# Kernel optimization log

Measured on AMD Instinct MI355X. Metric: run time of the kernel, lower is better.

## Reference

```python
import jax, jax.numpy as jnp
import numpy as np

NUM_HEADS = 16
HEAD_SIZE = 64
LN_EPS = 1e-5


def setup_inputs() -> dict:
    key = jax.random.key(0)
    k1, k2, k3 = jax.random.split(key, 3)
    b, l, hidden = 2, 2048, 1024
    qkv_out = HEAD_SIZE * NUM_HEADS + 2 * HEAD_SIZE  # 1152
    x = jax.random.normal(k1, (b, l, hidden), dtype=jnp.float32)
    Wqkv = jax.random.normal(k2, (qkv_out, hidden), dtype=jnp.float32) * 0.02
    gamma = jnp.ones((qkv_out,), dtype=jnp.float32)
    beta = jnp.zeros((qkv_out,), dtype=jnp.float32)
    Wfc = jax.random.normal(k3, (hidden, HEAD_SIZE * NUM_HEADS), dtype=jnp.float32) * 0.02
    return {"x": x, "Wqkv": Wqkv, "gamma": gamma, "beta": beta, "Wfc": Wfc}


def reference(x, Wqkv, gamma, beta, Wfc):
    h, d = NUM_HEADS, HEAD_SIZE
    b, l, _ = x.shape
    # fused QKV projection (no bias), then LayerNorm over the FULL qkv dim
    qkv = jnp.einsum('blc,oc->blo', x, Wqkv)  # (b, l, (h+2)*d)
    mu = jnp.mean(qkv, axis=-1, keepdims=True)
    var = jnp.var(qkv, axis=-1, keepdims=True)
    qkv = (qkv - mu) * jax.lax.rsqrt(var + LN_EPS) * gamma + beta
    qkv = qkv.reshape(b, l, h + 2, d)
    k = qkv[:, :, 0, :]       # (b, l, d) shared K head
    v = qkv[:, :, 1, :]       # (b, l, d) shared V head
    q = qkv[:, :, 2:, :]      # (b, l, h, d) query heads
    scale = 1.0 / np.sqrt(d).astype(np.float32)
    scores = jnp.einsum('bqhd,bkd->bhqk', q, k) * scale  # (b, h, l, l)
    causal = jnp.tril(jnp.ones((l, l), dtype=bool))
    scores = jnp.where(causal, scores, jnp.finfo(scores.dtype).min)
    attn = jax.nn.softmax(scores, axis=-1)
    out = jnp.einsum('bhqk,bkd->bqhd', attn, v).reshape(b, l, h * d)
    return jnp.einsum('blo,ho->blh', out, Wfc)
```

## Files before the change

kernel.cpp:

```cpp
#include <hip/hip_runtime.h>
#include <stdint.h>

typedef __attribute__((ext_vector_type(8))) short s16x8;
typedef __attribute__((ext_vector_type(4))) float f32x4;

#define MFMA16(a, b, c) __builtin_amdgcn_mfma_f32_16x16x32_bf16((a), (b), (c), 0, 0, 0)

__device__ __forceinline__ unsigned short f2bf(float f) {
    unsigned int u = __float_as_uint(f);
    return (unsigned short)((u + 0x7FFFu + ((u >> 16) & 1u)) >> 16);
}
__device__ __forceinline__ float bf2f(unsigned short h) {
    return __uint_as_float(((unsigned int)h) << 16);
}
__device__ __forceinline__ void cvt8(unsigned short* dst, const float* src) {
    const float4 f0 = *(const float4*)(src);
    const float4 f1 = *(const float4*)(src + 4);
    s16x8 v;
    v[0] = (short)f2bf(f0.x); v[1] = (short)f2bf(f0.y);
    v[2] = (short)f2bf(f0.z); v[3] = (short)f2bf(f0.w);
    v[4] = (short)f2bf(f1.x); v[5] = (short)f2bf(f1.y);
    v[6] = (short)f2bf(f1.z); v[7] = (short)f2bf(f1.w);
    *(s16x8*)dst = v;
}
__device__ __forceinline__ void gl_lds16(const unsigned short* g, unsigned short* l) {
    __builtin_amdgcn_global_load_lds(
        (const __attribute__((address_space(1))) unsigned int*)g,
        (__attribute__((address_space(3))) unsigned int*)l,
        16, 0, 0);
}

__global__ __launch_bounds__(256) void cvt_all(const float* __restrict__ x,
                                               const float* __restrict__ wq,
                                               const float* __restrict__ wf,
                                               unsigned short* __restrict__ xb,
                                               unsigned short* __restrict__ wqb,
                                               unsigned short* __restrict__ wfb) {
    const int blk = blockIdx.x;
    const float* src;
    unsigned short* dst;
    int base;
    if (blk < 2048)      { src = x;  dst = xb;  base = blk; }
    else if (blk < 2624) { src = wq; dst = wqb; base = blk - 2048; }
    else                 { src = wf; dst = wfb; base = blk - 2624; }
    const int i = (base * 256 + threadIdx.x) * 8;
    cvt8(&dst[i], &src[i]);
}

template <bool OUT_F32>
__global__ __launch_bounds__(256) void gemm_mn(const unsigned short* __restrict__ A,
                                               const unsigned short* __restrict__ Bw,
                                               void* __restrict__ Cout, int K, int N) {
    const int bm = blockIdx.x, bn = blockIdx.y;
    const int t = threadIdx.x;
    const int lane = t & 63, w = t >> 6;
    const int quad = lane >> 4, col = lane & 15;
    const int wm = (w >> 1) * 64, wn = (w & 1) * 32;

    __shared__ alignas(16) unsigned short As[128 * 64];
    __shared__ alignas(16) unsigned short Bs[64 * 64];

    f32x4 acc[4][2];
#pragma unroll
    for (int i = 0; i < 4; ++i)
#pragma unroll
        for (int j = 0; j < 2; ++j) acc[i][j] = (f32x4){0.f, 0.f, 0.f, 0.f};

    const int lrow = lane >> 3;
    const int lcol = (lane & 7) * 8;
    const unsigned short* Ap = A + (size_t)(bm * 128 + w * 8 + lrow) * K + lcol;
    const unsigned short* Bp = Bw + (size_t)(bn * 64 + w * 8 + lrow) * K + lcol;

    for (int k0 = 0; k0 < K; k0 += 64) {
        __syncthreads();
#pragma unroll
        for (int j = 0; j < 4; ++j)
            gl_lds16(Ap + (size_t)(j * 32) * K + k0, &As[(j * 32 + w * 8) * 64]);
#pragma unroll
        for (int j = 0; j < 2; ++j)
            gl_lds16(Bp + (size_t)(j * 32) * K + k0, &Bs[(j * 32 + w * 8) * 64]);
        __syncthreads();
#pragma unroll
        for (int s = 0; s < 2; ++s) {
            s16x8 af[4], bfr[2];
#pragma unroll
            for (int i = 0; i < 4; ++i)
                af[i] = *(const s16x8*)&As[(wm + i * 16 + col) * 64 + s * 32 + quad * 8];
#pragma unroll
            for (int j = 0; j < 2; ++j)
                bfr[j] = *(const s16x8*)&Bs[(wn + j * 16 + col) * 64 + s * 32 + quad * 8];
#pragma unroll
            for (int i = 0; i < 4; ++i)
#pragma unroll
                for (int j = 0; j < 2; ++j)
                    acc[i][j] = MFMA16(af[i], bfr[j], acc[i][j]);
        }
    }
    const int rowb = bm * 128 + wm + quad * 4;
    const int colb = bn * 64 + wn + col;
#pragma unroll
    for (int i = 0; i < 4; ++i)
#pragma unroll
        for (int j = 0; j < 2; ++j)
#pragma unroll
            for (int r = 0; r < 4; ++r) {
                size_t off = (size_t)(rowb + i * 16 + r) * N + colb + j * 16;
                if (OUT_F32) ((float*)Cout)[off] = acc[i][j][r];
                else ((unsigned short*)Cout)[off] = f2bf(acc[i][j][r]);
            }
}

__global__ __launch_bounds__(256) void ln_split(unsigned short* __restrict__ qkvn,
                                                const float* __restrict__ gamma,
                                                const float* __restrict__ beta,
                                                unsigned short* __restrict__ vT) {
    const int row = blockIdx.x;
    const int b = row >> 11, l = row & 2047;
    unsigned short* rp = qkvn + (size_t)row * 1152;
    const int t = threadIdx.x;
    const bool act = t < 144;

    float fv[8];
    float s = 0.f, s2 = 0.f;
    if (act) {
        s16x8 v = *(const s16x8*)&rp[t * 8];
#pragma unroll
        for (int e = 0; e < 8; ++e) {
            fv[e] = bf2f((unsigned short)v[e]);
            s += fv[e];
            s2 += fv[e] * fv[e];
        }
    } else {
#pragma unroll
        for (int e = 0; e < 8; ++e) fv[e] = 0.f;
    }
#pragma unroll
    for (int off = 32; off; off >>= 1) {
        s += __shfl_down(s, off);
        s2 += __shfl_down(s2, off);
    }
    __shared__ float red[8];
    const int lane = t & 63, w = t >> 6;
    if (lane == 0) { red[w] = s; red[w + 4] = s2; }
    __syncthreads();
    s = red[0] + red[1] + red[2] + red[3];
    s2 = red[4] + red[5] + red[6] + red[7];
    const float mu = s * (1.0f / 1152.0f);
    float var = s2 * (1.0f / 1152.0f) - mu * mu;
    var = fmaxf(var, 0.0f);
    const float rstd = rsqrtf(var + 1e-5f);

    if (act) {
        float4 g0 = *(const float4*)&gamma[t * 8];
        float4 g1 = *(const float4*)&gamma[t * 8 + 4];
        float4 e0 = *(const float4*)&beta[t * 8];
        float4 e1 = *(const float4*)&beta[t * 8 + 4];
        const float gg[8] = {g0.x, g0.y, g0.z, g0.w, g1.x, g1.y, g1.z, g1.w};
        const float bb[8] = {e0.x, e0.y, e0.z, e0.w, e1.x, e1.y, e1.z, e1.w};
        s16x8 o;
#pragma unroll
        for (int e = 0; e < 8; ++e)
            o[e] = (short)f2bf((fv[e] - mu) * rstd * gg[e] + bb[e]);
        *(s16x8*)&rp[t * 8] = o;
        if (t >= 8 && t < 16) {
            const int d0 = t * 8 - 64;
#pragma unroll
            for (int e = 0; e < 8; ++e)
                vT[((size_t)(b * 64 + d0 + e)) * 2048 + l] = (unsigned short)o[e];
        }
    }
}

__global__ __launch_bounds__(512) void attn_kernel(const unsigned short* __restrict__ qkvn,
                                                   const unsigned short* __restrict__ vT,
                                                   unsigned short* __restrict__ obuf) {
    const int b = blockIdx.x >> 3, hp = blockIdx.x & 7;
    const int qb = 31 - blockIdx.y;
    const int t = threadIdx.x;
    const int lane = t & 63, w = t >> 6;
    const int quad = lane >> 4, col = lane & 15;
    const int hl = w >> 2, wq = w & 3;

    __shared__ alignas(16) unsigned short Ks[2][64][72];
    __shared__ alignas(16) unsigned short Vts[2][64][72];
    __shared__ alignas(16) unsigned short PQ[8][16][72];

    unsigned short(*Qs)[72] = (unsigned short(*)[72])PQ;

    const int rs = t >> 3;
    const int cs = (t & 7) * 8;

#pragma unroll
    for (int hh = 0; hh < 2; ++hh) {
        const unsigned short* qsrc =
            qkvn + (size_t)(b * 2048 + qb * 64 + rs) * 1152 + 128 + (hp * 2 + hh) * 64 + cs;
        s16x8 v = *(const s16x8*)qsrc;
#pragma unroll
        for (int e = 0; e < 8; ++e)
            v[e] = (short)f2bf(bf2f((unsigned short)v[e]) * 0.125f);
        *(s16x8*)&Qs[hh * 64 + rs][cs] = v;
    }
    __syncthreads();
    const s16x8 qf0 = *(const s16x8*)&Qs[hl * 64 + wq * 16 + col][quad * 8];
    const s16x8 qf1 = *(const s16x8*)&Qs[hl * 64 + wq * 16 + col][32 + quad * 8];

    const unsigned short* kbase = qkvn + (size_t)(b * 2048 + rs) * 1152 + cs;
    const unsigned short* vbase = vT + (size_t)(b * 64 + rs) * 2048 + cs;
    *(uint4*)&Ks[0][rs][cs]  = *(const uint4*)(kbase);
    *(uint4*)&Vts[0][rs][cs] = *(const uint4*)(vbase);
    __syncthreads();

    s16x8 ones;
#pragma unroll
    for (int e = 0; e < 8; ++e) ones[e] = (short)0x3F80;

    f32x4 Oacc[4];
    f32x4 lacc = {0.f, 0.f, 0.f, 0.f};
#pragma unroll
    for (int nt = 0; nt < 4; ++nt) Oacc[nt] = (f32x4){0.f, 0.f, 0.f, 0.f};

    const int qg = qb * 64 + wq * 16 + quad * 4;

    for (int kb = 0; kb <= qb; ++kb) {
        const int p = kb & 1;
        uint4 kreg, vreg;
        if (kb < qb) {
            kreg = *(const uint4*)(kbase + (size_t)(kb + 1) * 64 * 1152);
            vreg = *(const uint4*)(vbase + (kb + 1) * 64);
        }

        f32x4 S[4];
#pragma unroll
        for (int nt = 0; nt < 4; ++nt) {
            s16x8 kf0 = *(const s16x8*)&Ks[p][nt * 16 + col][quad * 8];
            s16x8 kf1 = *(const s16x8*)&Ks[p][nt * 16 + col][32 + quad * 8];
            f32x4 z = (f32x4){0.f, 0.f, 0.f, 0.f};
            z = MFMA16(qf0, kf0, z);
            z = MFMA16(qf1, kf1, z);
            S[nt] = z;
        }
        if (kb == qb) {
#pragma unroll
            for (int nt = 0; nt < 4; ++nt)
#pragma unroll
                for (int r = 0; r < 4; ++r)
                    if (kb * 64 + nt * 16 + col > qg + r) S[nt][r] = -1e30f;
        }

#pragma unroll
        for (int nt = 0; nt < 4; ++nt)
#pragma unroll
            for (int r = 0; r < 4; ++r)
                PQ[w][quad * 4 + r][nt * 16 + col] = f2bf(__expf(S[nt][r] - 12.0f));

        const s16x8 pf0 = *(const s16x8*)&PQ[w][col][quad * 8];
        const s16x8 pf1 = *(const s16x8*)&PQ[w][col][32 + quad * 8];
        lacc = MFMA16(pf0, ones, lacc);
        lacc = MFMA16(pf1, ones, lacc);
#pragma unroll
        for (int nt = 0; nt < 4; ++nt) {
            s16x8 vf0 = *(const s16x8*)&Vts[p][nt * 16 + col][quad * 8];
            s16x8 vf1 = *(const s16x8*)&Vts[p][nt * 16 + col][32 + quad * 8];
            Oacc[nt] = MFMA16(pf0, vf0, Oacc[nt]);
            Oacc[nt] = MFMA16(pf1, vf1, Oacc[nt]);
        }

        if (kb < qb) {
            *(uint4*)&Ks[p ^ 1][rs][cs]  = kreg;
            *(uint4*)&Vts[p ^ 1][rs][cs] = vreg;
        }
        __syncthreads();
    }

    const int h = hp * 2 + hl;
#pragma unroll
    for (int r = 0; r < 4; ++r) {
        float inv = 1.0f / lacc[r];
        size_t base = (((size_t)b * 2048 + qg + r) * 16 + h) * 64;
#pragma unroll
        for (int nt = 0; nt < 4; ++nt)
            obuf[base + nt * 16 + col] = f2bf(Oacc[nt][r] * inv);
    }
}

extern "C" void kernel_launch(void* const* d_in, const int* in_sizes, int n_in,
                              void* d_out, int out_size, void* d_ws, size_t ws_size,
                              hipStream_t stream) {
    (void)in_sizes; (void)n_in; (void)out_size; (void)ws_size;
    const float* x     = (const float*)d_in[0];
    const float* Wqkv  = (const float*)d_in[1];
    const float* gamma = (const float*)d_in[2];
    const float* beta  = (const float*)d_in[3];
    const float* Wfc   = (const float*)d_in[4];
    float* out = (float*)d_out;

    char* ws = (char*)d_ws;
    unsigned short* xb   = (unsigned short*)ws;
    unsigned short* Wqb  = (unsigned short*)(ws + 8388608);
    unsigned short* Wfb  = (unsigned short*)(ws + 10747904);
    unsigned short* qkvn = (unsigned short*)(ws + 12845056);
    unsigned short* vT   = (unsigned short*)(ws + 22282240);
    unsigned short* abuf = (unsigned short*)ws;

    cvt_all<<<dim3(3136), 256, 0, stream>>>(x, Wqkv, Wfc, xb, Wqb, Wfb);
    gemm_mn<false><<<dim3(32, 18), 256, 0, stream>>>(xb, Wqb, qkvn, 1024, 1152);
    ln_split<<<dim3(4096), 256, 0, stream>>>(qkvn, gamma, beta, vT);
    attn_kernel<<<dim3(16, 32), 512, 0, stream>>>(qkvn, vT, abuf);
    gemm_mn<true><<<dim3(32, 16), 256, 0, stream>>>(abuf, Wfb, out, 1024, 1024);
}
```

Measured before the change: 172.7 us.

## Double-buffer GEMM LDS tiles and use single-wave LayerNorm rows

```diff
diff --git a/kernel.cpp b/kernel.cpp
--- a/kernel.cpp
+++ b/kernel.cpp
@@ -57,8 +57,8 @@
     const int quad = lane >> 4, col = lane & 15;
     const int wm = (w >> 1) * 64, wn = (w & 1) * 32;
 
-    __shared__ alignas(16) unsigned short As[128 * 64];
-    __shared__ alignas(16) unsigned short Bs[64 * 64];
+    __shared__ alignas(16) unsigned short As[2][128 * 64];
+    __shared__ alignas(16) unsigned short Bs[2][64 * 64];
 
     f32x4 acc[4][2];
 #pragma unroll
@@ -71,30 +71,40 @@
     const unsigned short* Ap = A + (size_t)(bm * 128 + w * 8 + lrow) * K + lcol;
     const unsigned short* Bp = Bw + (size_t)(bn * 64 + w * 8 + lrow) * K + lcol;
 
+#pragma unroll
+    for (int j = 0; j < 4; ++j)
+        gl_lds16(Ap + (size_t)(j * 32) * K, &As[0][(j * 32 + w * 8) * 64]);
+#pragma unroll
+    for (int j = 0; j < 2; ++j)
+        gl_lds16(Bp + (size_t)(j * 32) * K, &Bs[0][(j * 32 + w * 8) * 64]);
+    __syncthreads();
+
     for (int k0 = 0; k0 < K; k0 += 64) {
-        __syncthreads();
-#pragma unroll
-        for (int j = 0; j < 4; ++j)
-            gl_lds16(Ap + (size_t)(j * 32) * K + k0, &As[(j * 32 + w * 8) * 64]);
-#pragma unroll
-        for (int j = 0; j < 2; ++j)
-            gl_lds16(Bp + (size_t)(j * 32) * K + k0, &Bs[(j * 32 + w * 8) * 64]);
-        __syncthreads();
+        const int p = (k0 >> 6) & 1;
+        if (k0 + 64 < K) {
+#pragma unroll
+            for (int j = 0; j < 4; ++j)
+                gl_lds16(Ap + (size_t)(j * 32) * K + k0 + 64, &As[p ^ 1][(j * 32 + w * 8) * 64]);
+#pragma unroll
+            for (int j = 0; j < 2; ++j)
+                gl_lds16(Bp + (size_t)(j * 32) * K + k0 + 64, &Bs[p ^ 1][(j * 32 + w * 8) * 64]);
+        }
 #pragma unroll
         for (int s = 0; s < 2; ++s) {
             s16x8 af[4], bfr[2];
 #pragma unroll
             for (int i = 0; i < 4; ++i)
-                af[i] = *(const s16x8*)&As[(wm + i * 16 + col) * 64 + s * 32 + quad * 8];
+                af[i] = *(const s16x8*)&As[p][(wm + i * 16 + col) * 64 + s * 32 + quad * 8];
 #pragma unroll
             for (int j = 0; j < 2; ++j)
-                bfr[j] = *(const s16x8*)&Bs[(wn + j * 16 + col) * 64 + s * 32 + quad * 8];
+                bfr[j] = *(const s16x8*)&Bs[p][(wn + j * 16 + col) * 64 + s * 32 + quad * 8];
 #pragma unroll
             for (int i = 0; i < 4; ++i)
 #pragma unroll
                 for (int j = 0; j < 2; ++j)
                     acc[i][j] = MFMA16(af[i], bfr[j], acc[i][j]);
         }
+        __syncthreads();
     }
     const int rowb = bm * 128 + wm + quad * 4;
     const int colb = bn * 64 + wn + col;
@@ -110,64 +120,67 @@
             }
 }
 
-__global__ __launch_bounds__(256) void ln_split(unsigned short* __restrict__ qkvn,
-                                                const float* __restrict__ gamma,
-                                                const float* __restrict__ beta,
-                                                unsigned short* __restrict__ vT) {
+__global__ __launch_bounds__(64) void ln_row(unsigned short* __restrict__ qkvn,
+                                             const float* __restrict__ gamma,
+                                             const float* __restrict__ beta,
+                                             unsigned short* __restrict__ vT) {
     const int row = blockIdx.x;
     const int b = row >> 11, l = row & 2047;
     unsigned short* rp = qkvn + (size_t)row * 1152;
-    const int t = threadIdx.x;
-    const bool act = t < 144;
-
-    float fv[8];
+    const int lane = threadIdx.x;
+
+    s16x8 v0 = *(const s16x8*)&rp[lane * 8];
+    s16x8 v1 = *(const s16x8*)&rp[512 + lane * 8];
+    unsigned int v2u = *(const unsigned int*)&rp[1024 + lane * 2];
+
+    float f0[8], f1[8], f2[2];
     float s = 0.f, s2 = 0.f;
-    if (act) {
-        s16x8 v = *(const s16x8*)&rp[t * 8];
-#pragma unroll
-        for (int e = 0; e < 8; ++e) {
-            fv[e] = bf2f((unsigned short)v[e]);
-            s += fv[e];
-            s2 += fv[e] * fv[e];
-        }
-    } else {
-#pragma unroll
-        for (int e = 0; e < 8; ++e) fv[e] = 0.f;
-    }
-#pragma unroll
-    for (int off = 32; off; off >>= 1) {
-        s += __shfl_down(s, off);
-        s2 += __shfl_down(s2, off);
-    }
-    __shared__ float red[8];
-    const int lane = t & 63, w = t >> 6;
-    if (lane == 0) { red[w] = s; red[w + 4] = s2; }
-    __syncthreads();
-    s = red[0] + red[1] + red[2] + red[3];
-    s2 = red[4] + red[5] + red[6] + red[7];
+#pragma unroll
+    for (int e = 0; e < 8; ++e) {
+        f0[e] = bf2f((unsigned short)v0[e]);
+        f1[e] = bf2f((unsigned short)v1[e]);
+        s += f0[e] + f1[e];
+        s2 += f0[e] * f0[e] + f1[e] * f1[e];
+    }
+    f2[0] = bf2f((unsigned short)(v2u & 0xFFFF));
+    f2[1] = bf2f((unsigned short)(v2u >> 16));
+    s += f2[0] + f2[1];
+    s2 += f2[0] * f2[0] + f2[1] * f2[1];
+
+#pragma unroll
+    for (int off = 1; off < 64; off <<= 1) {
+        s += __shfl_xor(s, off);
+        s2 += __shfl_xor(s2, off);
+    }
     const float mu = s * (1.0f / 1152.0f);
     float var = s2 * (1.0f / 1152.0f) - mu * mu;
     var = fmaxf(var, 0.0f);
     const float rstd = rsqrtf(var + 1e-5f);
 
-    if (act) {
-        float4 g0 = *(const float4*)&gamma[t * 8];
-        float4 g1 = *(const float4*)&gamma[t * 8 + 4];
-        float4 e0 = *(const float4*)&beta[t * 8];
-        float4 e1 = *(const float4*)&beta[t * 8 + 4];
-        const float gg[8] = {g0.x, g0.y, g0.z, g0.w, g1.x, g1.y, g1.z, g1.w};
-        const float bb[8] = {e0.x, e0.y, e0.z, e0.w, e1.x, e1.y, e1.z, e1.w};
+    {
         s16x8 o;
 #pragma unroll
         for (int e = 0; e < 8; ++e)
-            o[e] = (short)f2bf((fv[e] - mu) * rstd * gg[e] + bb[e]);
-        *(s16x8*)&rp[t * 8] = o;
-        if (t >= 8 && t < 16) {
-            const int d0 = t * 8 - 64;
+            o[e] = (short)f2bf((f0[e] - mu) * rstd * gamma[lane * 8 + e] + beta[lane * 8 + e]);
+        *(s16x8*)&rp[lane * 8] = o;
+        if (lane >= 8 && lane < 16) {
+            const int d0 = lane * 8 - 64;
 #pragma unroll
             for (int e = 0; e < 8; ++e)
                 vT[((size_t)(b * 64 + d0 + e)) * 2048 + l] = (unsigned short)o[e];
         }
+    }
+    {
+        s16x8 o;
+#pragma unroll
+        for (int e = 0; e < 8; ++e)
+            o[e] = (short)f2bf((f1[e] - mu) * rstd * gamma[512 + lane * 8 + e] + beta[512 + lane * 8 + e]);
+        *(s16x8*)&rp[512 + lane * 8] = o;
+    }
+    {
+        unsigned short o0 = f2bf((f2[0] - mu) * rstd * gamma[1024 + lane * 2] + beta[1024 + lane * 2]);
+        unsigned short o1 = f2bf((f2[1] - mu) * rstd * gamma[1025 + lane * 2] + beta[1025 + lane * 2]);
+        *(unsigned int*)&rp[1024 + lane * 2] = ((unsigned int)o1 << 16) | o0;
     }
 }
 
@@ -304,7 +317,7 @@
 
     cvt_all<<<dim3(3136), 256, 0, stream>>>(x, Wqkv, Wfc, xb, Wqb, Wfb);
     gemm_mn<false><<<dim3(32, 18), 256, 0, stream>>>(xb, Wqb, qkvn, 1024, 1152);
-    ln_split<<<dim3(4096), 256, 0, stream>>>(qkvn, gamma, beta, vT);
+    ln_row<<<dim3(4096), 64, 0, stream>>>(qkvn, gamma, beta, vT);
     attn_kernel<<<dim3(16, 32), 512, 0, stream>>>(qkvn, vT, abuf);
     gemm_mn<true><<<dim3(32, 16), 256, 0, stream>>>(abuf, Wfb, out, 1024, 1024);
 }
```

Result: no change. 173.0 us (+0.1%).
